# Kernel tuning notes

Hardware: AMD Instinct MI355X
Metric: run time of the kernel (lower is better)

The kernel has to match this reference:

```python
import jax, jax.numpy as jnp
import numpy as np

N = 8192
D = 512
N_SLICE = 64
K = 8
H = 30 * K  # 240


def _gen_k_slice(rng):
    xx = rng.normal(0.0, 1.0, (N_SLICE, K, D))
    slices = np.zeros((N_SLICE, K, D), dtype=np.float64)
    for i in range(N_SLICE):
        _, _, vh = np.linalg.svd(xx[i], full_matrices=False)
        slices[i] = vh
    return slices.astype(np.float32)


def setup_inputs() -> dict:
    key = jax.random.key(0)
    k1, k2, k3, k4, k5, k6, k7 = jax.random.split(key, 7)
    rng = np.random.default_rng(0)
    # conv weights: PyTorch Conv1d default init ~ U(-s, s), s = 1/sqrt(fan_in)
    s1 = 1.0 / np.sqrt(K)
    s3 = 1.0 / np.sqrt(H)
    return {
        "X": jax.random.normal(k1, (N, D), dtype=jnp.float32),
        "Y": jax.random.normal(k2, (N, D), dtype=jnp.float32),
        "X_noise": jax.random.normal(k3, (N, N_SLICE * K), dtype=jnp.float32),
        "thetas": jnp.asarray(_gen_k_slice(rng)),                     # [S, K, D]
        "W1": jax.random.uniform(k4, (N_SLICE, H, K), jnp.float32, -s1, s1),
        "b1": jax.random.uniform(k5, (N_SLICE, H), jnp.float32, -s1, s1),
        "W3": jax.random.uniform(k6, (N_SLICE, H), jnp.float32, -s3, s3),
        "b3": jax.random.uniform(k7, (N_SLICE,), jnp.float32, -s3, s3),
        "sigma_noise": 0,
    }


def _mlp(sample, W1, b1, W3, b3):
    # sample: [N, S, K] -> grouped 1x1 conv k->H, relu, grouped conv H->1
    h1 = jax.nn.relu(jnp.einsum('nsk,shk->nsh', sample, W1) + b1[None])
    return jnp.einsum('nsh,sh->ns', h1, W3) + b3[None]  # [N, S]


def reference(X, Y, X_noise, thetas, W1, b1, W3, b3, sigma_noise):
    # batched per-slice projections (fuses the n_slice matmul loop)
    x_sample = jnp.einsum('nd,skd->nsk', X, thetas)  # [N, S, K]
    y_sample = jnp.einsum('nd,skd->nsk', Y, thetas)
    if sigma_noise > 0:
        x_sample = x_sample + sigma_noise * X_noise.reshape(X.shape[0], N_SLICE, K)
    pred_x = _mlp(x_sample, W1, b1, W3, b3)  # [N, S]
    pred_y = _mlp(y_sample, W1, b1, W3, b3)
    n_y = pred_y.shape[0]
    ret = jnp.mean(pred_x, axis=0) - jax.nn.logsumexp(
        pred_y - jnp.log(jnp.float32(n_y)), axis=0)
    return jnp.mean(-ret)
```

## Files before the change

kernel.cpp:

```cpp
#include <hip/hip_runtime.h>
#include <hip/hip_bf16.h>

#define NROWS 8192
#define DDIM  512
#define NS    64
#define KK    8
#define HH    240
#define LDT   40
#define SP2   72
#define BUF   (64 * LDT)

typedef __attribute__((ext_vector_type(8))) _Float16 f16x8;
typedef __attribute__((ext_vector_type(4))) _Float16 f16x4;
typedef __attribute__((ext_vector_type(4))) float f32x4;
typedef __attribute__((ext_vector_type(2))) float f32x2;

__device__ inline unsigned pk2u(float a, float b) {
    auto h = __builtin_amdgcn_cvt_pkrtz(a, b);
    unsigned u;
    __builtin_memcpy(&u, &h, sizeof(u));
    return u;
}

__global__ __launch_bounds__(256)
void pack_kernel(const float* __restrict__ W1, const float* __restrict__ Th,
                 ushort* __restrict__ W1h, ushort* __restrict__ Thh)
{
    int i = (blockIdx.x * 256 + threadIdx.x) * 4;
    if (i < 122880) {
        float4 v = *(const float4*)(W1 + i);
        *(uint2*)(W1h + i) = make_uint2(pk2u(v.x, v.y), pk2u(v.z, v.w));
    } else {
        int j = i - 122880;
        float4 v = *(const float4*)(Th + j);
        *(uint2*)(Thh + j) = make_uint2(pk2u(v.x, v.y), pk2u(v.z, v.w));
    }
}

__global__ __launch_bounds__(256, 4)
void proj_mlp_kernel(const float* __restrict__ X,
                     const float* __restrict__ Y,
                     const float* __restrict__ Xn,
                     const ushort* __restrict__ Thh,
                     const ushort* __restrict__ W1h,
                     const float* __restrict__ b1,
                     const float* __restrict__ W3,
                     const float* __restrict__ sig_p,
                     float* __restrict__ sumx,
                     float* __restrict__ maxy,
                     float* __restrict__ sey)
{
    __shared__ __align__(16) ushort smem[4 * BUF];
    ushort* sl = smem;

    const int tid  = threadIdx.x;
    const int w    = __builtin_amdgcn_readfirstlane(tid >> 6);
    const int lane = tid & 63;
    const int bx   = blockIdx.x;
    const int by   = blockIdx.y;

    const bool isX = (bx < 128);
    const int  bxl = isX ? bx : (bx - 128);
    const float*  srcA = (isX ? X : Y) + (size_t)bxl * 64 * DDIM;
    const ushort* srcB = Thh + (size_t)by * 64 * DDIM;

    f32x4 acc[2][2];
#pragma unroll
    for (int m = 0; m < 2; ++m)
#pragma unroll
        for (int n = 0; n < 2; ++n) acc[m][n] = (f32x4){0.f, 0.f, 0.f, 0.f};

    const int wr  = (w >> 1) * 32;
    const int wc  = (w & 1) * 32;
    const int r16 = lane & 15;
    const int hi4 = lane >> 4;
    const int offA = (wr + r16) * LDT + hi4 * 8;
    const int offB = (wc + r16) * LDT + hi4 * 8;

    const int arow0 = tid >> 3,  ac4 = tid & 7;
    const int brow  = tid >> 2,  bh  = tid & 3;

    float4 ra[2];
    uint4  rbv;

#define LOADA(k0) { _Pragma("unroll") \
    for (int i = 0; i < 2; ++i) \
        ra[i] = *(const float4*)(srcA + (size_t)(arow0 + i * 32) * DDIM + (k0) + ac4 * 4); }
#define LOADB(k0) \
    rbv = *(const uint4*)(srcB + brow * DDIM + (k0) + bh * 8);
#define STORE(buf) { ushort* aw_ = smem + (buf) * 2 * BUF; \
    _Pragma("unroll") \
    for (int i = 0; i < 2; ++i) \
        *(uint2*)(aw_ + (arow0 + i * 32) * LDT + ac4 * 4) = \
            make_uint2(pk2u(ra[i].x, ra[i].y), pk2u(ra[i].z, ra[i].w)); \
    *(uint4*)(aw_ + BUF + brow * LDT + bh * 8) = rbv; }

    LOADA(0); LOADB(0);
    STORE(0);
    LOADA(32); LOADB(32);
    __syncthreads();

#pragma unroll 2
    for (int kt = 0; kt < 16; ++kt) {
        const int cur = kt & 1;
        const ushort* aT = smem + cur * 2 * BUF;
        const ushort* bT = aT + BUF;

        f16x8 af[2], bfv[2];
#pragma unroll
        for (int m = 0; m < 2; ++m) {
            af[m]  = *(const f16x8*)(aT + offA + m * 16 * LDT);
            bfv[m] = *(const f16x8*)(bT + offB + m * 16 * LDT);
        }
#pragma unroll
        for (int m = 0; m < 2; ++m)
#pragma unroll
            for (int n = 0; n < 2; ++n)
                acc[m][n] = __builtin_amdgcn_mfma_f32_16x16x32_f16(
                    af[m], bfv[n], acc[m][n], 0, 0, 0);

        if (kt < 15) STORE(cur ^ 1);
        if (kt < 14) { LOADA((kt + 2) * 32); LOADB((kt + 2) * 32); }
        __syncthreads();
    }

    const float sig = *sig_p;
    const bool addnoise = (sig > 0.f) && isX;
    const int n0g = bxl * 64;

#pragma unroll
    for (int m = 0; m < 2; ++m)
#pragma unroll
        for (int n = 0; n < 2; ++n) {
            const int col  = wc + n * 16 + r16;
            const int rowb = wr + m * 16 + hi4 * 4;
            float v[4];
#pragma unroll
            for (int j = 0; j < 4; ++j) {
                v[j] = acc[m][n][j];
                if (addnoise)
                    v[j] = fmaf(sig, Xn[(size_t)(n0g + rowb + j) * (NS * KK) + by * 64 + col], v[j]);
            }
            unsigned u01 = pk2u(v[0], v[1]);
            unsigned u23 = pk2u(v[2], v[3]);
            sl[(rowb + 0) * SP2 + col] = (ushort)u01;
            sl[(rowb + 1) * SP2 + col] = (ushort)(u01 >> 16);
            sl[(rowb + 2) * SP2 + col] = (ushort)u23;
            sl[(rowb + 3) * SP2 + col] = (ushort)(u23 >> 16);
        }
    __syncthreads();

#pragma unroll 1
    for (int si = 0; si < 2; ++si) {
        const int sloc = w * 2 + si;
        const int s    = by * 8 + sloc;

        f16x4 bsamp[4];
#pragma unroll
        for (int nt = 0; nt < 4; ++nt) {
            f16x4 t = {0, 0, 0, 0};
            if (hi4 < 2)
                t = *(const f16x4*)(sl + (nt * 16 + r16) * SP2 + sloc * 8 + hi4 * 4);
            bsamp[nt] = t;
        }

        const ushort* w1p = W1h + (size_t)s * HH * KK;
        const float*  b1p = b1 + s * HH;
        const float*  w3p = W3 + s * HH;

        f32x2 pn2[4];
#pragma unroll
        for (int nt = 0; nt < 4; ++nt) pn2[nt] = (f32x2){0.f, 0.f};

#pragma unroll 5
        for (int ht = 0; ht < HH / 16; ++ht) {
            f16x4 aw = {0, 0, 0, 0};
            if (hi4 < 2)
                aw = *(const f16x4*)(w1p + (ht * 16 + r16) * 8 + hi4 * 4);
            float4 b4 = *(const float4*)(b1p + ht * 16 + hi4 * 4);
            float4 w4 = *(const float4*)(w3p + ht * 16 + hi4 * 4);
            f32x4 z   = (f32x4){b4.x, b4.y, b4.z, b4.w};
            f32x2 w01 = (f32x2){w4.x, w4.y};
            f32x2 w23 = (f32x2){w4.z, w4.w};
            const f32x2 zero2 = (f32x2){0.f, 0.f};
#pragma unroll
            for (int nt = 0; nt < 4; ++nt) {
                f32x4 t = __builtin_amdgcn_mfma_f32_16x16x16f16(aw, bsamp[nt], z, 0, 0, 0);
                f32x2 t01 = (f32x2){t[0], t[1]};
                f32x2 t23 = (f32x2){t[2], t[3]};
                t01 = __builtin_elementwise_max(t01, zero2);
                t23 = __builtin_elementwise_max(t23, zero2);
                pn2[nt] = __builtin_elementwise_fma(t01, w01, pn2[nt]);
                pn2[nt] = __builtin_elementwise_fma(t23, w23, pn2[nt]);
            }
        }

        if (isX) {
            float lsum = 0.f;
#pragma unroll
            for (int nt = 0; nt < 4; ++nt) lsum += pn2[nt].x + pn2[nt].y;
#pragma unroll
            for (int off = 1; off < 64; off <<= 1)
                lsum += __shfl_xor(lsum, off);
            if (lane == 0) sumx[s * 128 + bxl] = lsum;
        } else {
            float p[4];
#pragma unroll
            for (int nt = 0; nt < 4; ++nt) {
                f32x2 v = pn2[nt];
                v.x += __shfl_xor(v.x, 16);
                v.y += __shfl_xor(v.y, 16);
                v.x += __shfl_xor(v.x, 32);
                v.y += __shfl_xor(v.y, 32);
                p[nt] = v.x + v.y;
            }
            float M = fmaxf(fmaxf(p[0], p[1]), fmaxf(p[2], p[3]));
            float se = __expf(p[0] - M) + __expf(p[1] - M)
                     + __expf(p[2] - M) + __expf(p[3] - M);
#pragma unroll
            for (int off = 1; off < 16; off <<= 1) {
                float Mo = __shfl_xor(M, off);
                float so = __shfl_xor(se, off);
                float Mm = fmaxf(M, Mo);
                se = se * __expf(M - Mm) + so * __expf(Mo - Mm);
                M = Mm;
            }
            if (lane == 0) {
                maxy[s * 128 + bxl] = M;
                sey[s * 128 + bxl]  = se;
            }
        }
    }
}

__global__ __launch_bounds__(256)
void final_kernel(const float* __restrict__ sumx,
                  const float* __restrict__ maxy,
                  const float* __restrict__ sey,
                  float* __restrict__ out)
{
    __shared__ float term_s[NS];
    const int tid = threadIdx.x;
    const int s = tid >> 2, q = tid & 3;
    const int base = s * 128 + q * 32;

    float sum = 0.f, M = -3.4e38f;
#pragma unroll 8
    for (int i = 0; i < 32; ++i) {
        sum += sumx[base + i];
        M = fmaxf(M, maxy[base + i]);
    }
    float se = 0.f;
#pragma unroll 8
    for (int i = 0; i < 32; ++i)
        se += sey[base + i] * __expf(maxy[base + i] - M);

#pragma unroll
    for (int off = 1; off < 4; off <<= 1) {
        float Mo = __shfl_xor(M, off);
        float so = __shfl_xor(se, off);
        float su = __shfl_xor(sum, off);
        float Mm = fmaxf(M, Mo);
        se = se * __expf(M - Mm) + so * __expf(Mo - Mm);
        M = Mm;
        sum += su;
    }
    if (q == 0)
        term_s[s] = M + logf(se) - logf((float)NROWS) - sum * (1.0f / (float)NROWS);
    __syncthreads();
    if (tid < 64) {
        float v = term_s[tid];
#pragma unroll
        for (int off = 1; off < 64; off <<= 1) v += __shfl_xor(v, off);
        if (tid == 0) out[0] = v * (1.0f / (float)NS);
    }
}

extern "C" void kernel_launch(void* const* d_in, const int* in_sizes, int n_in,
                              void* d_out, int out_size, void* d_ws, size_t ws_size,
                              hipStream_t stream)
{
    const float* X   = (const float*)d_in[0];
    const float* Y   = (const float*)d_in[1];
    const float* Xn  = (const float*)d_in[2];
    const float* Th  = (const float*)d_in[3];
    const float* W1  = (const float*)d_in[4];
    const float* b1  = (const float*)d_in[5];
    const float* W3  = (const float*)d_in[6];
    const float* sig = (const float*)d_in[8];

    ushort* W1h  = (ushort*)d_ws;
    ushort* Thh  = W1h + 122880;
    float*  sumx = (float*)(Thh + 262144);
    float*  maxy = sumx + NS * 128;
    float*  sey  = maxy + NS * 128;

    pack_kernel<<<(122880 + 262144) / 1024, 256, 0, stream>>>(W1, Th, W1h, Thh);

    dim3 g1(256, 8, 1);
    proj_mlp_kernel<<<g1, 256, 0, stream>>>(X, Y, Xn, Thh, W1h, b1, W3,
                                            sig, sumx, maxy, sey);
    final_kernel<<<1, 256, 0, stream>>>(sumx, maxy, sey, (float*)d_out);
}
```

Measured before the change: 68.67 us.

## Widen projection tile to 128 theta columns per block to halve X/Y rereads

Each block now projects a 64-row slab of X or Y against 128 theta rows (16 slices) instead of 64, with a 2x4 MFMA accumulator grid per wave. The grid's y-dimension halves, so the fp32 X/Y matrices are streamed from memory half as many times. Each wave then runs the per-slice MLP for 4 slices instead of 2. The shared-memory stores for the next k-tile are also moved ahead of the MFMA work in the loop. The trade-off is more accumulator registers, a larger LDS footprint and fewer blocks to spread across the GPU.

Result: slower. 89.98 us (+31.0%).

```diff
diff --git a/kernel.cpp b/kernel.cpp
--- a/kernel.cpp
+++ b/kernel.cpp
@@ -7,8 +7,10 @@
 #define KK    8
 #define HH    240
 #define LDT   40
-#define SP2   72
-#define BUF   (64 * LDT)
+#define SP    136
+#define ABUF  (64 * LDT)
+#define BBUF  (128 * LDT)
+#define STAGE1 (ABUF + BBUF)
 
 typedef __attribute__((ext_vector_type(8))) _Float16 f16x8;
 typedef __attribute__((ext_vector_type(4))) _Float16 f16x4;
@@ -50,7 +52,7 @@
                      float* __restrict__ maxy,
                      float* __restrict__ sey)
 {
-    __shared__ __align__(16) ushort smem[4 * BUF];
+    __shared__ __align__(16) ushort smem[2 * STAGE1];
     ushort* sl = smem;
 
     const int tid  = threadIdx.x;
@@ -62,38 +64,42 @@
     const bool isX = (bx < 128);
     const int  bxl = isX ? bx : (bx - 128);
     const float*  srcA = (isX ? X : Y) + (size_t)bxl * 64 * DDIM;
-    const ushort* srcB = Thh + (size_t)by * 64 * DDIM;
-
-    f32x4 acc[2][2];
+    const ushort* srcB = Thh + (size_t)by * 128 * DDIM;
+
+    f32x4 acc[2][4];
 #pragma unroll
     for (int m = 0; m < 2; ++m)
 #pragma unroll
-        for (int n = 0; n < 2; ++n) acc[m][n] = (f32x4){0.f, 0.f, 0.f, 0.f};
+        for (int n = 0; n < 4; ++n) acc[m][n] = (f32x4){0.f, 0.f, 0.f, 0.f};
 
     const int wr  = (w >> 1) * 32;
-    const int wc  = (w & 1) * 32;
+    const int wc  = (w & 1) * 64;
     const int r16 = lane & 15;
     const int hi4 = lane >> 4;
     const int offA = (wr + r16) * LDT + hi4 * 8;
     const int offB = (wc + r16) * LDT + hi4 * 8;
 
-    const int arow0 = tid >> 3,  ac4 = tid & 7;
-    const int brow  = tid >> 2,  bh  = tid & 3;
+    const int ar = tid >> 3, ac4 = tid & 7;
+    const int br = tid >> 2, bc  = tid & 3;
 
     float4 ra[2];
-    uint4  rbv;
+    uint4  rbv[2];
 
 #define LOADA(k0) { _Pragma("unroll") \
     for (int i = 0; i < 2; ++i) \
-        ra[i] = *(const float4*)(srcA + (size_t)(arow0 + i * 32) * DDIM + (k0) + ac4 * 4); }
-#define LOADB(k0) \
-    rbv = *(const uint4*)(srcB + brow * DDIM + (k0) + bh * 8);
-#define STORE(buf) { ushort* aw_ = smem + (buf) * 2 * BUF; \
+        ra[i] = *(const float4*)(srcA + (size_t)(ar + i * 32) * DDIM + (k0) + ac4 * 4); }
+#define LOADB(k0) { _Pragma("unroll") \
+    for (int i = 0; i < 2; ++i) \
+        rbv[i] = *(const uint4*)(srcB + (size_t)(br + i * 64) * DDIM + (k0) + bc * 8); }
+#define STORE(buf) { ushort* aw_ = smem + (buf) * STAGE1; \
     _Pragma("unroll") \
     for (int i = 0; i < 2; ++i) \
-        *(uint2*)(aw_ + (arow0 + i * 32) * LDT + ac4 * 4) = \
+        *(uint2*)(aw_ + (ar + i * 32) * LDT + ac4 * 4) = \
             make_uint2(pk2u(ra[i].x, ra[i].y), pk2u(ra[i].z, ra[i].w)); \
-    *(uint4*)(aw_ + BUF + brow * LDT + bh * 8) = rbv; }
+    ushort* bw_ = aw_ + ABUF; \
+    _Pragma("unroll") \
+    for (int i = 0; i < 2; ++i) \
+        *(uint4*)(bw_ + (br + i * 64) * LDT + bc * 8) = rbv[i]; }
 
     LOADA(0); LOADB(0);
     STORE(0);
@@ -103,24 +109,24 @@
 #pragma unroll 2
     for (int kt = 0; kt < 16; ++kt) {
         const int cur = kt & 1;
-        const ushort* aT = smem + cur * 2 * BUF;
-        const ushort* bT = aT + BUF;
-
-        f16x8 af[2], bfv[2];
-#pragma unroll
-        for (int m = 0; m < 2; ++m) {
-            af[m]  = *(const f16x8*)(aT + offA + m * 16 * LDT);
-            bfv[m] = *(const f16x8*)(bT + offB + m * 16 * LDT);
-        }
+
+        if (kt < 15) STORE(cur ^ 1);
+        if (kt < 14) { LOADA((kt + 2) * 32); LOADB((kt + 2) * 32); }
+
+        const ushort* aT = smem + cur * STAGE1;
+        const ushort* bT = aT + ABUF;
+        f16x8 af[2], bfv[4];
+#pragma unroll
+        for (int m = 0; m < 2; ++m) af[m] = *(const f16x8*)(aT + offA + m * 16 * LDT);
+#pragma unroll
+        for (int n = 0; n < 4; ++n) bfv[n] = *(const f16x8*)(bT + offB + n * 16 * LDT);
 #pragma unroll
         for (int m = 0; m < 2; ++m)
 #pragma unroll
-            for (int n = 0; n < 2; ++n)
+            for (int n = 0; n < 4; ++n)
                 acc[m][n] = __builtin_amdgcn_mfma_f32_16x16x32_f16(
                     af[m], bfv[n], acc[m][n], 0, 0, 0);
 
-        if (kt < 15) STORE(cur ^ 1);
-        if (kt < 14) { LOADA((kt + 2) * 32); LOADB((kt + 2) * 32); }
         __syncthreads();
     }
 
@@ -131,7 +137,7 @@
 #pragma unroll
     for (int m = 0; m < 2; ++m)
 #pragma unroll
-        for (int n = 0; n < 2; ++n) {
+        for (int n = 0; n < 4; ++n) {
             const int col  = wc + n * 16 + r16;
             const int rowb = wr + m * 16 + hi4 * 4;
             float v[4];
@@ -139,28 +145,28 @@
             for (int j = 0; j < 4; ++j) {
                 v[j] = acc[m][n][j];
                 if (addnoise)
-                    v[j] = fmaf(sig, Xn[(size_t)(n0g + rowb + j) * (NS * KK) + by * 64 + col], v[j]);
+                    v[j] = fmaf(sig, Xn[(size_t)(n0g + rowb + j) * (NS * KK) + by * 128 + col], v[j]);
             }
             unsigned u01 = pk2u(v[0], v[1]);
             unsigned u23 = pk2u(v[2], v[3]);
-            sl[(rowb + 0) * SP2 + col] = (ushort)u01;
-            sl[(rowb + 1) * SP2 + col] = (ushort)(u01 >> 16);
-            sl[(rowb + 2) * SP2 + col] = (ushort)u23;
-            sl[(rowb + 3) * SP2 + col] = (ushort)(u23 >> 16);
+            sl[(rowb + 0) * SP + col] = (ushort)u01;
+            sl[(rowb + 1) * SP + col] = (ushort)(u01 >> 16);
+            sl[(rowb + 2) * SP + col] = (ushort)u23;
+            sl[(rowb + 3) * SP + col] = (ushort)(u23 >> 16);
         }
     __syncthreads();
 
 #pragma unroll 1
-    for (int si = 0; si < 2; ++si) {
-        const int sloc = w * 2 + si;
-        const int s    = by * 8 + sloc;
+    for (int si = 0; si < 4; ++si) {
+        const int sloc = w * 4 + si;
+        const int s    = by * 16 + sloc;
 
         f16x4 bsamp[4];
 #pragma unroll
         for (int nt = 0; nt < 4; ++nt) {
             f16x4 t = {0, 0, 0, 0};
             if (hi4 < 2)
-                t = *(const f16x4*)(sl + (nt * 16 + r16) * SP2 + sloc * 8 + hi4 * 4);
+                t = *(const f16x4*)(sl + (nt * 16 + r16) * SP + sloc * 8 + hi4 * 4);
             bsamp[nt] = t;
         }
 
@@ -297,7 +303,7 @@
 
     pack_kernel<<<(122880 + 262144) / 1024, 256, 0, stream>>>(W1, Th, W1h, Thh);
 
-    dim3 g1(256, 8, 1);
+    dim3 g1(256, 4, 1);
     proj_mlp_kernel<<<g1, 256, 0, stream>>>(X, Y, Xn, Thh, W1h, b1, W3,
                                             sig, sumx, maxy, sey);
     final_kernel<<<1, 256, 0, stream>>>(sumx, maxy, sey, (float*)d_out);
```

## Pre-convert X/Y to fp16 and stream GEMM tiles via direct global-to-LDS loads

Applied to the files above, without the earlier changes.

The pack kernel now also converts X and Y to fp16 in workspace, in addition to Theta and W1. The projection GEMM then loads fp16 tiles straight into an XOR-swizzled, double-buffered LDS layout using global_load_lds, replacing register staging, in-kernel fp32-to-fp16 conversion and the padded LDS stride. The aim is to halve the bytes the GEMM re-reads across the eight slice-group blocks and to cut VGPR and VALU work in the main loop. In exchange it adds a full extra read and write pass over X and Y, and it shrinks the shared buffer, which later MLP-phase code may rely on.

Result: faster. 67.32 us (-2.0%).

```diff
diff --git a/kernel.cpp b/kernel.cpp
--- a/kernel.cpp
+++ b/kernel.cpp
@@ -6,14 +6,15 @@
 #define NS    64
 #define KK    8
 #define HH    240
-#define LDT   40
 #define SP2   72
-#define BUF   (64 * LDT)
 
 typedef __attribute__((ext_vector_type(8))) _Float16 f16x8;
 typedef __attribute__((ext_vector_type(4))) _Float16 f16x4;
 typedef __attribute__((ext_vector_type(4))) float f32x4;
 typedef __attribute__((ext_vector_type(2))) float f32x2;
+
+typedef __attribute__((address_space(3))) void       lds_void;
+typedef const __attribute__((address_space(1))) void gbl_cvoid;
 
 __device__ inline unsigned pk2u(float a, float b) {
     auto h = __builtin_amdgcn_cvt_pkrtz(a, b);
@@ -22,24 +23,30 @@
     return u;
 }
 
+__device__ inline void gl16(const ushort* g, ushort* l) {
+    __builtin_amdgcn_global_load_lds((gbl_cvoid*)g, (lds_void*)l, 16, 0, 0);
+}
+
+#define XN (NROWS * DDIM)
 __global__ __launch_bounds__(256)
-void pack_kernel(const float* __restrict__ W1, const float* __restrict__ Th,
-                 ushort* __restrict__ W1h, ushort* __restrict__ Thh)
+void pack_kernel(const float* __restrict__ X, const float* __restrict__ Y,
+                 const float* __restrict__ Th, const float* __restrict__ W1,
+                 ushort* __restrict__ Xh, ushort* __restrict__ Yh,
+                 ushort* __restrict__ Thh, ushort* __restrict__ W1h)
 {
     int i = (blockIdx.x * 256 + threadIdx.x) * 4;
-    if (i < 122880) {
-        float4 v = *(const float4*)(W1 + i);
-        *(uint2*)(W1h + i) = make_uint2(pk2u(v.x, v.y), pk2u(v.z, v.w));
-    } else {
-        int j = i - 122880;
-        float4 v = *(const float4*)(Th + j);
-        *(uint2*)(Thh + j) = make_uint2(pk2u(v.x, v.y), pk2u(v.z, v.w));
-    }
+    const float* src; ushort* dst; int off;
+    if (i < XN)               { src = X;  dst = Xh;  off = i; }
+    else if (i < 2 * XN)      { src = Y;  dst = Yh;  off = i - XN; }
+    else if (i < 2 * XN + 262144) { src = Th; dst = Thh; off = i - 2 * XN; }
+    else                      { src = W1; dst = W1h; off = i - (2 * XN + 262144); }
+    float4 v = *(const float4*)(src + off);
+    *(uint2*)(dst + off) = make_uint2(pk2u(v.x, v.y), pk2u(v.z, v.w));
 }
 
 __global__ __launch_bounds__(256, 4)
-void proj_mlp_kernel(const float* __restrict__ X,
-                     const float* __restrict__ Y,
+void proj_mlp_kernel(const ushort* __restrict__ Xh,
+                     const ushort* __restrict__ Yh,
                      const float* __restrict__ Xn,
                      const ushort* __restrict__ Thh,
                      const ushort* __restrict__ W1h,
@@ -50,7 +57,7 @@
                      float* __restrict__ maxy,
                      float* __restrict__ sey)
 {
-    __shared__ __align__(16) ushort smem[4 * BUF];
+    __shared__ __align__(16) ushort smem[8192];
     ushort* sl = smem;
 
     const int tid  = threadIdx.x;
@@ -61,8 +68,13 @@
 
     const bool isX = (bx < 128);
     const int  bxl = isX ? bx : (bx - 128);
-    const float*  srcA = (isX ? X : Y) + (size_t)bxl * 64 * DDIM;
-    const ushort* srcB = Thh + (size_t)by * 64 * DDIM;
+    const ushort* srcA = (isX ? Xh : Yh) + (size_t)bxl * 64 * DDIM;
+
+    const int grow = (w << 4) + (lane >> 2);
+    const int gchk = (lane & 3) ^ ((grow >> 1) & 3);
+    const ushort* gA = srcA + (size_t)grow * DDIM + gchk * 8;
+    const ushort* gB = Thh + (size_t)(by * 64 + grow) * DDIM + gchk * 8;
+    const int woff = w * 512;
 
     f32x4 acc[2][2];
 #pragma unroll
@@ -74,53 +86,42 @@
     const int wc  = (w & 1) * 32;
     const int r16 = lane & 15;
     const int hi4 = lane >> 4;
-    const int offA = (wr + r16) * LDT + hi4 * 8;
-    const int offB = (wc + r16) * LDT + hi4 * 8;
-
-    const int arow0 = tid >> 3,  ac4 = tid & 7;
-    const int brow  = tid >> 2,  bh  = tid & 3;
-
-    float4 ra[2];
-    uint4  rbv;
-
-#define LOADA(k0) { _Pragma("unroll") \
-    for (int i = 0; i < 2; ++i) \
-        ra[i] = *(const float4*)(srcA + (size_t)(arow0 + i * 32) * DDIM + (k0) + ac4 * 4); }
-#define LOADB(k0) \
-    rbv = *(const uint4*)(srcB + brow * DDIM + (k0) + bh * 8);
-#define STORE(buf) { ushort* aw_ = smem + (buf) * 2 * BUF; \
-    _Pragma("unroll") \
-    for (int i = 0; i < 2; ++i) \
-        *(uint2*)(aw_ + (arow0 + i * 32) * LDT + ac4 * 4) = \
-            make_uint2(pk2u(ra[i].x, ra[i].y), pk2u(ra[i].z, ra[i].w)); \
-    *(uint4*)(aw_ + BUF + brow * LDT + bh * 8) = rbv; }
-
-    LOADA(0); LOADB(0);
-    STORE(0);
-    LOADA(32); LOADB(32);
+
+    int offA[2], offB[2];
+#pragma unroll
+    for (int m = 0; m < 2; ++m) {
+        int row = wr + m * 16 + r16;
+        offA[m] = row * 32 + ((hi4 ^ ((row >> 1) & 3)) * 8);
+    }
+#pragma unroll
+    for (int n = 0; n < 2; ++n) {
+        int row = wc + n * 16 + r16;
+        offB[n] = 2048 + row * 32 + ((hi4 ^ ((row >> 1) & 3)) * 8);
+    }
+
+    gl16(gA, &smem[woff]);
+    gl16(gB, &smem[2048 + woff]);
     __syncthreads();
 
-#pragma unroll 2
+#pragma unroll
     for (int kt = 0; kt < 16; ++kt) {
-        const int cur = kt & 1;
-        const ushort* aT = smem + cur * 2 * BUF;
-        const ushort* bT = aT + BUF;
-
+        const int cur = (kt & 1) * 4096;
+        if (kt < 15) {
+            const int nxt = 4096 - cur;
+            gl16(gA + (kt + 1) * 32, &smem[nxt + woff]);
+            gl16(gB + (kt + 1) * 32, &smem[nxt + 2048 + woff]);
+        }
         f16x8 af[2], bfv[2];
 #pragma unroll
-        for (int m = 0; m < 2; ++m) {
-            af[m]  = *(const f16x8*)(aT + offA + m * 16 * LDT);
-            bfv[m] = *(const f16x8*)(bT + offB + m * 16 * LDT);
-        }
+        for (int m = 0; m < 2; ++m) af[m]  = *(const f16x8*)(smem + cur + offA[m]);
+#pragma unroll
+        for (int n = 0; n < 2; ++n) bfv[n] = *(const f16x8*)(smem + cur + offB[n]);
 #pragma unroll
         for (int m = 0; m < 2; ++m)
 #pragma unroll
             for (int n = 0; n < 2; ++n)
                 acc[m][n] = __builtin_amdgcn_mfma_f32_16x16x32_f16(
                     af[m], bfv[n], acc[m][n], 0, 0, 0);
-
-        if (kt < 15) STORE(cur ^ 1);
-        if (kt < 14) { LOADA((kt + 2) * 32); LOADB((kt + 2) * 32); }
         __syncthreads();
     }
 
@@ -289,16 +290,19 @@
     const float* W3  = (const float*)d_in[6];
     const float* sig = (const float*)d_in[8];
 
-    ushort* W1h  = (ushort*)d_ws;
-    ushort* Thh  = W1h + 122880;
-    float*  sumx = (float*)(Thh + 262144);
+    ushort* Xh   = (ushort*)d_ws;
+    ushort* Yh   = Xh + XN;
+    ushort* Thh  = Yh + XN;
+    ushort* W1h  = Thh + 262144;
+    float*  sumx = (float*)(W1h + 122880);
     float*  maxy = sumx + NS * 128;
     float*  sey  = maxy + NS * 128;
 
-    pack_kernel<<<(122880 + 262144) / 1024, 256, 0, stream>>>(W1, Th, W1h, Thh);
+    pack_kernel<<<(2 * XN + 262144 + 122880) / 1024, 256, 0, stream>>>(
+        X, Y, Th, W1, Xh, Yh, Thh, W1h);
 
     dim3 g1(256, 8, 1);
-    proj_mlp_kernel<<<g1, 256, 0, stream>>>(X, Y, Xn, Thh, W1h, b1, W3,
+    proj_mlp_kernel<<<g1, 256, 0, stream>>>(Xh, Yh, Xn, Thh, W1h, b1, W3,
                                             sig, sumx, maxy, sey);
     final_kernel<<<1, 256, 0, stream>>>(sumx, maxy, sey, (float*)d_out);
 }
```
